# Kernel tuning notes

Hardware: AMD Instinct MI355X
Metric: run time of the kernel (lower is better)

## Reference

```python
import jax, jax.numpy as jnp
import numpy as np

N_NODES = 20000
N_EDGES = 640000
B = 256
GNN_DIM = 256
HID = 512
INNER = 2048
RANK = 512
N_CLASSES = 3
N_GENES = 6640


def _ln(x, s, b, eps=1e-5):
    mu = jnp.mean(x, axis=-1, keepdims=True)
    var = jnp.mean(jnp.square(x - mu), axis=-1, keepdims=True)
    return (x - mu) * jax.lax.rsqrt(var + eps) * s + b


def setup_inputs() -> dict:
    key = jax.random.key(0)
    ks = jax.random.split(key, 16)
    s = 0.02
    return {
        "node_indices": jax.random.randint(ks[0], (B,), 0, N_NODES, dtype=jnp.int32),
        "edge_index": jax.random.randint(ks[1], (2, N_EDGES), 0, N_NODES, dtype=jnp.int32),
        "edge_weight": jax.random.uniform(ks[2], (N_EDGES,), dtype=jnp.float32),
        "partial_emb": jax.random.normal(ks[3], (N_NODES, GNN_DIM), dtype=jnp.float32),
        "oov_emb": jnp.zeros((1, GNN_DIM), jnp.float32),
        "gnn_ln_s": jnp.ones((3, GNN_DIM), jnp.float32),
        "gnn_ln_b": jnp.zeros((3, GNN_DIM), jnp.float32),
        "gnn_w": jax.random.normal(ks[4], (3, GNN_DIM, GNN_DIM), jnp.float32) * s,
        "gnn_b": jnp.zeros((3, GNN_DIM), jnp.float32),
        "post_w": jax.random.normal(ks[5], (GNN_DIM, GNN_DIM), jnp.float32) * s,
        "post_b": jnp.zeros((GNN_DIM,), jnp.float32),
        "pin_w": jax.random.normal(ks[6], (GNN_DIM, HID), jnp.float32) * s,
        "pin_b": jnp.zeros((HID,), jnp.float32),
        "blk_ln_s": jnp.ones((6, HID), jnp.float32),
        "blk_ln_b": jnp.zeros((6, HID), jnp.float32),
        "blk_w1": jax.random.normal(ks[7], (6, HID, INNER), jnp.float32) * s,
        "blk_b1": jnp.zeros((6, INNER), jnp.float32),
        "blk_w2": jax.random.normal(ks[8], (6, INNER, HID), jnp.float32) * s,
        "blk_b2": jnp.zeros((6, HID), jnp.float32),
        "pout_w": jax.random.normal(ks[9], (HID, N_CLASSES * RANK), jnp.float32) * s,
        "pout_b": jnp.zeros((N_CLASSES * RANK,), jnp.float32),
        "out_gene_emb": jax.random.normal(ks[10], (N_GENES, RANK), jnp.float32) * s,
    }


def reference(node_indices, edge_index, edge_weight, partial_emb, oov_emb,
              gnn_ln_s, gnn_ln_b, gnn_w, gnn_b, post_w, post_b,
              pin_w, pin_b, blk_ln_s, blk_ln_b, blk_w1, blk_b1, blk_w2, blk_b2,
              pout_w, pout_b, out_gene_emb):
    n = partial_emb.shape[0]
    src, dst = edge_index[0], edge_index[1]
    # --- trainable GNN tail: 3 layers of (LN -> weighted scatter-sum -> Linear -> ReLU) + residual ---
    x = partial_emb
    for i in range(3):
        h = _ln(x, gnn_ln_s[i], gnn_ln_b[i])
        msg = h[src] * edge_weight[:, None]              # [E, 256] gather (memory-bound)
        agg = jax.ops.segment_sum(msg, dst, num_segments=n)
        h = jax.nn.relu(agg @ gnn_w[i] + gnn_b[i])
        x = h + x
    x = x @ post_w + post_b                              # post_mp
    # --- OOV-safe perturbation embedding lookup ---
    oov = node_indices < 0
    safe = jnp.where(oov, 0, node_indices)
    pert = jnp.where(oov[:, None], oov_emb, x[safe])     # [B, 256]
    # --- bilinear head ---
    h = pert @ pin_w + pin_b
    for i in range(6):
        z = _ln(h, blk_ln_s[i], blk_ln_b[i])
        z = jax.nn.gelu(z @ blk_w1[i] + blk_b1[i], approximate=False)
        h = h + z @ blk_w2[i] + blk_b2[i]                # dropout = identity (eval)
    proj = (h @ pout_w + pout_b).reshape(h.shape[0], N_CLASSES, RANK)
    logits = jnp.einsum('bcr,gr->bcg', proj, out_gene_emb)
    return logits
```

## Files before the change

### kernel.cpp

```cpp
#include <hip/hip_runtime.h>
#include <hip/hip_bf16.h>
#include <math.h>

#define NNODES 20000
#define NEDGES 640000
#define BSZ 256
#define GDIM 256
#define HID 512
#define INNER 2048
#define RANK 512
#define NCLS 3
#define NGENES 6640

typedef __attribute__((ext_vector_type(8))) short bf16x8;
typedef __attribute__((ext_vector_type(4))) float f32x4;

__device__ inline float bf2f(unsigned short u) {
    return __uint_as_float(((unsigned)u) << 16);
}
__device__ inline unsigned short f2bf(float f) {
    unsigned u = __float_as_uint(f);
    u = u + 0x7fff + ((u >> 16) & 1);
    return (unsigned short)(u >> 16);
}

__global__ void hist_k(const int* __restrict__ dst, int* __restrict__ counts, int E) {
    int e = blockIdx.x * 256 + threadIdx.x;
    if (e < E) atomicAdd(&counts[dst[e]], 1);
}

__global__ void scan1_k(const int* __restrict__ counts, int* __restrict__ incl,
                        int* __restrict__ bsums, int n) {
    __shared__ int s[256];
    int i = blockIdx.x * 256 + threadIdx.x;
    int v = (i < n) ? counts[i] : 0;
    s[threadIdx.x] = v;
    __syncthreads();
    for (int off = 1; off < 256; off <<= 1) {
        int t = (threadIdx.x >= off) ? s[threadIdx.x - off] : 0;
        __syncthreads();
        s[threadIdx.x] += t;
        __syncthreads();
    }
    if (i < n) incl[i] = s[threadIdx.x];
    if (threadIdx.x == 255) bsums[blockIdx.x] = s[255];
}

__global__ void scan2_k(const int* __restrict__ bsums, int* __restrict__ boffs, int nb) {
    __shared__ int s[128];
    int tid = threadIdx.x;
    int v = (tid < nb) ? bsums[tid] : 0;
    s[tid] = v;
    __syncthreads();
    for (int off = 1; off < 128; off <<= 1) {
        int t = (tid >= off) ? s[tid - off] : 0;
        __syncthreads();
        s[tid] += t;
        __syncthreads();
    }
    if (tid < nb) boffs[tid] = s[tid] - v;
}

__global__ void scan3_k(const int* __restrict__ incl, const int* __restrict__ counts,
                        const int* __restrict__ boffs, int* __restrict__ row_start,
                        int* __restrict__ cursor, int n) {
    int i = blockIdx.x * 256 + threadIdx.x;
    if (i < n) {
        int st = incl[i] - counts[i] + boffs[blockIdx.x];
        row_start[i] = st;
        cursor[i] = st;
    }
}

__global__ void scatter_k(const int* __restrict__ src, const int* __restrict__ dst,
                          const float* __restrict__ w, int* __restrict__ cursor,
                          int2* __restrict__ ep, int E) {
    int e = blockIdx.x * 256 + threadIdx.x;
    if (e < E) {
        int d = dst[e];
        int p = atomicAdd(&cursor[d], 1);
        ep[p] = make_int2(src[e], __float_as_int(w[e]));
    }
}

__global__ void cvtb_k(const float* __restrict__ X, unsigned short* __restrict__ Y, int n8) {
    int i = blockIdx.x * 256 + threadIdx.x;
    if (i >= n8) return;
    const float4* xp = (const float4*)X;
    float4 a = xp[i * 2], b = xp[i * 2 + 1];
    *(ushort4*)(Y + (size_t)i * 8) = make_ushort4(f2bf(a.x), f2bf(a.y), f2bf(a.z), f2bf(a.w));
    *(ushort4*)(Y + (size_t)i * 8 + 4) = make_ushort4(f2bf(b.x), f2bf(b.y), f2bf(b.z), f2bf(b.w));
}

__global__ void tconv_k(const float* __restrict__ W, unsigned short* __restrict__ WT, int K,
                        int N) {
    __shared__ float s[32][33];
    const float* Wl = W + (size_t)blockIdx.z * K * N;
    unsigned short* WTl = WT + (size_t)blockIdx.z * K * N;
    int k0 = blockIdx.y * 32, n0 = blockIdx.x * 32;
#pragma unroll
    for (int i = 0; i < 4; i++)
        s[threadIdx.y + 8 * i][threadIdx.x] =
            Wl[(size_t)(k0 + threadIdx.y + 8 * i) * N + n0 + threadIdx.x];
    __syncthreads();
#pragma unroll
    for (int i = 0; i < 4; i++)
        WTl[(size_t)(n0 + threadIdx.y + 8 * i) * K + k0 + threadIdx.x] =
            f2bf(s[threadIdx.x][threadIdx.y + 8 * i]);
}

__global__ void lnb_k(const float* __restrict__ X, const float* __restrict__ sc,
                      const float* __restrict__ bi, unsigned short* __restrict__ Y, int M) {
    int row = blockIdx.x * 4 + (threadIdx.x >> 6);
    int lane = threadIdx.x & 63;
    if (row >= M) return;
    float4 v = ((const float4*)(X + (size_t)row * GDIM))[lane];
    float sum = v.x + v.y + v.z + v.w;
#pragma unroll
    for (int off = 32; off >= 1; off >>= 1) sum += __shfl_xor(sum, off);
    float mu = sum / GDIM;
    float a = v.x - mu, b = v.y - mu, c = v.z - mu, d = v.w - mu;
    float sq = a * a + b * b + c * c + d * d;
#pragma unroll
    for (int off = 32; off >= 1; off >>= 1) sq += __shfl_xor(sq, off);
    float rstd = rsqrtf(sq / GDIM + 1e-5f);
    float4 s4 = ((const float4*)sc)[lane];
    float4 b4 = ((const float4*)bi)[lane];
    *(ushort4*)(Y + (size_t)row * GDIM + lane * 4) =
        make_ushort4(f2bf(a * rstd * s4.x + b4.x), f2bf(b * rstd * s4.y + b4.y),
                     f2bf(c * rstd * s4.z + b4.z), f2bf(d * rstd * s4.w + b4.w));
}

__device__ inline void agg_row(int beg, int cnt, int lane, const int2* __restrict__ ep,
                               const unsigned short* __restrict__ H, float& a0, float& a1,
                               float& a2, float& a3) {
    int t = 0;
    for (; t + 16 <= cnt; t += 16) {
        int2 e[16];
#pragma unroll
        for (int u = 0; u < 16; u++) e[u] = ep[beg + t + u];
        ushort4 v[16];
#pragma unroll
        for (int u = 0; u < 16; u++)
            v[u] = *(const ushort4*)(H + (size_t)e[u].x * GDIM + lane * 4);
#pragma unroll
        for (int u = 0; u < 16; u++) {
            float w = __int_as_float(e[u].y);
            a0 = fmaf(bf2f(v[u].x), w, a0);
            a1 = fmaf(bf2f(v[u].y), w, a1);
            a2 = fmaf(bf2f(v[u].z), w, a2);
            a3 = fmaf(bf2f(v[u].w), w, a3);
        }
    }
    for (; t + 4 <= cnt; t += 4) {
        int2 e[4];
#pragma unroll
        for (int u = 0; u < 4; u++) e[u] = ep[beg + t + u];
        ushort4 v[4];
#pragma unroll
        for (int u = 0; u < 4; u++)
            v[u] = *(const ushort4*)(H + (size_t)e[u].x * GDIM + lane * 4);
#pragma unroll
        for (int u = 0; u < 4; u++) {
            float w = __int_as_float(e[u].y);
            a0 = fmaf(bf2f(v[u].x), w, a0);
            a1 = fmaf(bf2f(v[u].y), w, a1);
            a2 = fmaf(bf2f(v[u].z), w, a2);
            a3 = fmaf(bf2f(v[u].w), w, a3);
        }
    }
    for (; t < cnt; t++) {
        int2 e = ep[beg + t];
        float w = __int_as_float(e.y);
        ushort4 v = *(const ushort4*)(H + (size_t)e.x * GDIM + lane * 4);
        a0 = fmaf(bf2f(v.x), w, a0);
        a1 = fmaf(bf2f(v.y), w, a1);
        a2 = fmaf(bf2f(v.z), w, a2);
        a3 = fmaf(bf2f(v.w), w, a3);
    }
}

__global__ void aggb_k(const int* __restrict__ row_start, const int* __restrict__ counts,
                       const int2* __restrict__ ep, const unsigned short* __restrict__ H,
                       unsigned short* __restrict__ AGG, int n) {
    int row = blockIdx.x * 4 + (threadIdx.x >> 6);
    int lane = threadIdx.x & 63;
    if (row >= n) return;
    float a0 = 0.f, a1 = 0.f, a2 = 0.f, a3 = 0.f;
    agg_row(row_start[row], counts[row], lane, ep, H, a0, a1, a2, a3);
    *(ushort4*)(AGG + (size_t)row * GDIM + lane * 4) =
        make_ushort4(f2bf(a0), f2bf(a1), f2bf(a2), f2bf(a3));
}

__global__ void aggsel_k(const int* __restrict__ idx, const int* __restrict__ row_start,
                         const int* __restrict__ counts, const int2* __restrict__ ep,
                         const unsigned short* __restrict__ H, unsigned short* __restrict__ AGG) {
    int b = blockIdx.x * 4 + (threadIdx.x >> 6);
    int lane = threadIdx.x & 63;
    int id = idx[b];
    int row = id < 0 ? 0 : id;
    float a0 = 0.f, a1 = 0.f, a2 = 0.f, a3 = 0.f;
    agg_row(row_start[row], counts[row], lane, ep, H, a0, a1, a2, a3);
    *(ushort4*)(AGG + (size_t)b * GDIM + lane * 4) =
        make_ushort4(f2bf(a0), f2bf(a1), f2bf(a2), f2bf(a3));
}

template <int ACT, bool RES, bool BIAS>
__global__ __launch_bounds__(256) void mgemm_k(const unsigned short* __restrict__ A,
                                               const unsigned short* __restrict__ BT,
                                               const float* __restrict__ bias,
                                               const float* __restrict__ R,
                                               float* __restrict__ C, int M, int N, int K) {
    __shared__ unsigned short As[128 * 32];
    __shared__ unsigned short Bs[128 * 32];
    int m0 = blockIdx.y * 128, n0 = blockIdx.x * 128;
    int tid = threadIdx.x;
    int wave = tid >> 6, lane = tid & 63;
    int wm = (wave >> 1) * 64, wn = (wave & 1) * 64;
    int lrow = lane & 15, lq = lane >> 4;

    f32x4 acc[4][4];
    const f32x4 zz = {0.f, 0.f, 0.f, 0.f};
#pragma unroll
    for (int i = 0; i < 4; i++)
#pragma unroll
        for (int j = 0; j < 4; j++) acc[i][j] = zz;

    int r0 = tid >> 2;
    int q = tid & 3;

    for (int k0 = 0; k0 < K; k0 += 32) {
#pragma unroll
        for (int p = 0; p < 2; p++) {
            int row = r0 + p * 64;
            int gm = m0 + row;
            uint4 va = make_uint4(0, 0, 0, 0);
            if (gm < M) va = *(const uint4*)(A + (size_t)gm * K + k0 + q * 8);
            *(uint4*)&As[row * 32 + q * 8] = va;
            int gn = n0 + row;
            uint4 vb = make_uint4(0, 0, 0, 0);
            if (gn < N) vb = *(const uint4*)(BT + (size_t)gn * K + k0 + q * 8);
            *(uint4*)&Bs[row * 32 + q * 8] = vb;
        }
        __syncthreads();
        bf16x8 af[4], bf[4];
#pragma unroll
        for (int i = 0; i < 4; i++)
            af[i] = *(const bf16x8*)&As[(wm + i * 16 + lrow) * 32 + lq * 8];
#pragma unroll
        for (int j = 0; j < 4; j++)
            bf[j] = *(const bf16x8*)&Bs[(wn + j * 16 + lrow) * 32 + lq * 8];
#pragma unroll
        for (int i = 0; i < 4; i++)
#pragma unroll
            for (int j = 0; j < 4; j++)
                acc[i][j] =
                    __builtin_amdgcn_mfma_f32_16x16x32_bf16(af[i], bf[j], acc[i][j], 0, 0, 0);
        __syncthreads();
    }

#pragma unroll
    for (int i = 0; i < 4; i++) {
#pragma unroll
        for (int j = 0; j < 4; j++) {
            int gn = n0 + wn + j * 16 + lrow;
            if (gn >= N) continue;
            float bv = BIAS ? bias[gn] : 0.f;
#pragma unroll
            for (int r = 0; r < 4; r++) {
                int gm = m0 + wm + i * 16 + lq * 4 + r;
                if (gm >= M) continue;
                float v = acc[i][j][r] + bv;
                if (ACT == 1) v = fmaxf(v, 0.f);
                if (RES) v += R[(size_t)gm * N + gn];
                C[(size_t)gm * N + gn] = v;
            }
        }
    }
}

template <int ACT, int EPI>
__global__ __launch_bounds__(256) void mfull_k(const unsigned short* __restrict__ A,
                                               const unsigned short* __restrict__ BT,
                                               const float* __restrict__ bias,
                                               const int* __restrict__ idx,
                                               const float* __restrict__ aux,
                                               unsigned short* __restrict__ O, int M, int N,
                                               int K) {
    __shared__ unsigned short As[64 * 32];
    __shared__ unsigned short Bs[64 * 32];
    int m0 = blockIdx.y * 64, n0 = blockIdx.x * 64;
    int tid = threadIdx.x;
    int wave = tid >> 6, lane = tid & 63;
    int wm = wave * 16;
    int lrow = lane & 15, lq = lane >> 4;
    f32x4 acc[4];
    const f32x4 zz = {0.f, 0.f, 0.f, 0.f};
#pragma unroll
    for (int j = 0; j < 4; j++) acc[j] = zz;
    int r0 = tid >> 2;
    int q = tid & 3;
    for (int k0 = 0; k0 < K; k0 += 32) {
        *(uint4*)&As[r0 * 32 + q * 8] = *(const uint4*)(A + (size_t)(m0 + r0) * K + k0 + q * 8);
        *(uint4*)&Bs[r0 * 32 + q * 8] = *(const uint4*)(BT + (size_t)(n0 + r0) * K + k0 + q * 8);
        __syncthreads();
        bf16x8 af = *(const bf16x8*)&As[(wm + lrow) * 32 + lq * 8];
#pragma unroll
        for (int j = 0; j < 4; j++) {
            bf16x8 bfr = *(const bf16x8*)&Bs[(j * 16 + lrow) * 32 + lq * 8];
            acc[j] = __builtin_amdgcn_mfma_f32_16x16x32_bf16(af, bfr, acc[j], 0, 0, 0);
        }
        __syncthreads();
    }
#pragma unroll
    for (int j = 0; j < 4; j++) {
        int gn = n0 + j * 16 + lrow;
        float bv = bias[gn];
#pragma unroll
        for (int r = 0; r < 4; r++) {
            int gm = m0 + wm + lq * 4 + r;
            float v = acc[j][r] + bv;
            if (ACT == 1) v = fmaxf(v, 0.f);
            if (ACT == 2) v = 0.5f * v * (1.f + erff(v * 0.70710678118654752f));
            if (EPI == 2) {
                int id = idx[gm];
                int safe = id < 0 ? 0 : id;
                v += aux[(size_t)safe * N + gn];
            }
            if (EPI == 1) {
                if (idx[gm] < 0) v = aux[gn];
            }
            O[(size_t)gm * N + gn] = f2bf(v);
        }
    }
}

__global__ __launch_bounds__(256) void msk_k(const unsigned short* __restrict__ A,
                                             const unsigned short* __restrict__ BT,
                                             float* __restrict__ Cp, int M, int N, int K,
                                             int kchunk) {
    __shared__ unsigned short As[64 * 32];
    __shared__ unsigned short Bs[64 * 32];
    int m0 = blockIdx.y * 64, n0 = blockIdx.x * 64;
    int kbeg = blockIdx.z * kchunk;
    float* C = Cp + (size_t)blockIdx.z * M * N;
    int tid = threadIdx.x;
    int wave = tid >> 6, lane = tid & 63;
    int wm = wave * 16;
    int lrow = lane & 15, lq = lane >> 4;
    f32x4 acc[4];
    const f32x4 zz = {0.f, 0.f, 0.f, 0.f};
#pragma unroll
    for (int j = 0; j < 4; j++) acc[j] = zz;
    int r0 = tid >> 2;
    int q = tid & 3;
    for (int k0 = kbeg; k0 < kbeg + kchunk; k0 += 32) {
        *(uint4*)&As[r0 * 32 + q * 8] = *(const uint4*)(A + (size_t)(m0 + r0) * K + k0 + q * 8);
        *(uint4*)&Bs[r0 * 32 + q * 8] = *(const uint4*)(BT + (size_t)(n0 + r0) * K + k0 + q * 8);
        __syncthreads();
        bf16x8 af = *(const bf16x8*)&As[(wm + lrow) * 32 + lq * 8];
#pragma unroll
        for (int j = 0; j < 4; j++) {
            bf16x8 bfr = *(const bf16x8*)&Bs[(j * 16 + lrow) * 32 + lq * 8];
            acc[j] = __builtin_amdgcn_mfma_f32_16x16x32_bf16(af, bfr, acc[j], 0, 0, 0);
        }
        __syncthreads();
    }
#pragma unroll
    for (int j = 0; j < 4; j++) {
        int gn = n0 + j * 16 + lrow;
#pragma unroll
        for (int r = 0; r < 4; r++) {
            int gm = m0 + wm + lq * 4 + r;
            C[(size_t)gm * N + gn] = acc[j][r];
        }
    }
}

template <bool RESID, bool DO_LN>
__global__ void redln_k(const float* __restrict__ Cp, const float* __restrict__ bias,
                        const float* __restrict__ ln_s, const float* __restrict__ ln_b,
                        float* __restrict__ hbuf, unsigned short* __restrict__ outbf, int S) {
    int row = blockIdx.x * 4 + (threadIdx.x >> 6);
    int lane = threadIdx.x & 63;
    float4 a0 = {0.f, 0.f, 0.f, 0.f}, a1 = a0;
    for (int s = 0; s < S; s++) {
        const float4* pp = (const float4*)(Cp + ((size_t)s * BSZ + row) * HID);
        float4 b0 = pp[lane * 2], b1 = pp[lane * 2 + 1];
        a0.x += b0.x; a0.y += b0.y; a0.z += b0.z; a0.w += b0.w;
        a1.x += b1.x; a1.y += b1.y; a1.z += b1.z; a1.w += b1.w;
    }
    const float4* bb = (const float4*)bias;
    float4 c0 = bb[lane * 2], c1 = bb[lane * 2 + 1];
    a0.x += c0.x; a0.y += c0.y; a0.z += c0.z; a0.w += c0.w;
    a1.x += c1.x; a1.y += c1.y; a1.z += c1.z; a1.w += c1.w;
    float4* hp = (float4*)(hbuf + (size_t)row * HID);
    if (RESID) {
        float4 r0 = hp[lane * 2], r1 = hp[lane * 2 + 1];
        a0.x += r0.x; a0.y += r0.y; a0.z += r0.z; a0.w += r0.w;
        a1.x += r1.x; a1.y += r1.y; a1.z += r1.z; a1.w += r1.w;
    }
    hp[lane * 2] = a0;
    hp[lane * 2 + 1] = a1;
    unsigned short* op = outbf + (size_t)row * HID;
    if (DO_LN) {
        float sum = a0.x + a0.y + a0.z + a0.w + a1.x + a1.y + a1.z + a1.w;
#pragma unroll
        for (int off = 32; off >= 1; off >>= 1) sum += __shfl_xor(sum, off);
        float mu = sum / HID;
        float d0 = a0.x - mu, d1 = a0.y - mu, d2 = a0.z - mu, d3 = a0.w - mu;
        float d4 = a1.x - mu, d5 = a1.y - mu, d6 = a1.z - mu, d7 = a1.w - mu;
        float sq = d0 * d0 + d1 * d1 + d2 * d2 + d3 * d3 + d4 * d4 + d5 * d5 + d6 * d6 + d7 * d7;
#pragma unroll
        for (int off = 32; off >= 1; off >>= 1) sq += __shfl_xor(sq, off);
        float rstd = rsqrtf(sq / HID + 1e-5f);
        const float4* sp = (const float4*)ln_s;
        const float4* bp = (const float4*)ln_b;
        float4 s0 = sp[lane * 2], s1 = sp[lane * 2 + 1];
        float4 t0 = bp[lane * 2], t1 = bp[lane * 2 + 1];
        *(ushort4*)(op + lane * 8) =
            make_ushort4(f2bf(d0 * rstd * s0.x + t0.x), f2bf(d1 * rstd * s0.y + t0.y),
                         f2bf(d2 * rstd * s0.z + t0.z), f2bf(d3 * rstd * s0.w + t0.w));
        *(ushort4*)(op + lane * 8 + 4) =
            make_ushort4(f2bf(d4 * rstd * s1.x + t1.x), f2bf(d5 * rstd * s1.y + t1.y),
                         f2bf(d6 * rstd * s1.z + t1.z), f2bf(d7 * rstd * s1.w + t1.w));
    } else {
        *(ushort4*)(op + lane * 8) = make_ushort4(f2bf(a0.x), f2bf(a0.y), f2bf(a0.z), f2bf(a0.w));
        *(ushort4*)(op + lane * 8 + 4) =
            make_ushort4(f2bf(a1.x), f2bf(a1.y), f2bf(a1.z), f2bf(a1.w));
    }
}

extern "C" void kernel_launch(void* const* d_in, const int* in_sizes, int n_in,
                              void* d_out, int out_size, void* d_ws, size_t ws_size,
                              hipStream_t stream) {
    const int* node_indices = (const int*)d_in[0];
    const int* edge_src = (const int*)d_in[1];
    const int* edge_dst = edge_src + NEDGES;
    const float* edge_w = (const float*)d_in[2];
    const float* partial_emb = (const float*)d_in[3];
    const float* oov_emb = (const float*)d_in[4];
    const float* gnn_ln_s = (const float*)d_in[5];
    const float* gnn_ln_b = (const float*)d_in[6];
    const float* gnn_w = (const float*)d_in[7];
    const float* gnn_b = (const float*)d_in[8];
    const float* post_w = (const float*)d_in[9];
    const float* post_b = (const float*)d_in[10];
    const float* pin_w = (const float*)d_in[11];
    const float* pin_b = (const float*)d_in[12];
    const float* blk_ln_s = (const float*)d_in[13];
    const float* blk_ln_b = (const float*)d_in[14];
    const float* blk_w1 = (const float*)d_in[15];
    const float* blk_b1 = (const float*)d_in[16];
    const float* blk_w2 = (const float*)d_in[17];
    const float* blk_b2 = (const float*)d_in[18];
    const float* pout_w = (const float*)d_in[19];
    const float* pout_b = (const float*)d_in[20];
    const float* gene = (const float*)d_in[21];
    float* out = (float*)d_out;

    char* p = (char*)d_ws;
    auto alloc = [&](size_t bytes) {
        char* r = p;
        p += (bytes + 255) & ~(size_t)255;
        return r;
    };
    int* counts = (int*)alloc(NNODES * 4);
    int* incl = (int*)alloc(NNODES * 4);
    int* bsums = (int*)alloc(128 * 4);
    int* boffs = (int*)alloc(128 * 4);
    int* row_start = (int*)alloc(NNODES * 4);
    int* cursor = (int*)alloc(NNODES * 4);
    int2* epack = (int2*)alloc((size_t)NEDGES * 8);
    float* part = (float*)alloc((size_t)NNODES * GDIM * 4);
    unsigned short* ln_bf = (unsigned short*)part;
    unsigned short* aggbf = (unsigned short*)((char*)part + (size_t)NNODES * GDIM * 2);
    float* xa = (float*)alloc((size_t)NNODES * GDIM * 4);
    float* xb = (float*)alloc((size_t)NNODES * GDIM * 4);
    float* hbuf = (float*)alloc((size_t)BSZ * HID * 4);
    unsigned short* aggselb = (unsigned short*)alloc((size_t)BSZ * GDIM * 2);
    unsigned short* pertinbf = (unsigned short*)alloc((size_t)BSZ * GDIM * 2);
    unsigned short* pertbf = (unsigned short*)alloc((size_t)BSZ * GDIM * 2);
    unsigned short* zlnbf = (unsigned short*)alloc((size_t)BSZ * HID * 2);
    unsigned short* z1bf = (unsigned short*)alloc((size_t)BSZ * INNER * 2);
    unsigned short* hbufbf = (unsigned short*)alloc((size_t)BSZ * HID * 2);
    unsigned short* projb = (unsigned short*)alloc((size_t)BSZ * NCLS * RANK * 2);
    unsigned short* gnnT = (unsigned short*)alloc((size_t)3 * GDIM * GDIM * 2);
    unsigned short* postT = (unsigned short*)alloc((size_t)GDIM * GDIM * 2);
    unsigned short* pinT = (unsigned short*)alloc((size_t)HID * GDIM * 2);
    unsigned short* w1T = (unsigned short*)alloc((size_t)6 * INNER * HID * 2);
    unsigned short* w2T = (unsigned short*)alloc((size_t)6 * HID * INNER * 2);
    unsigned short* poutT = (unsigned short*)alloc((size_t)NCLS * RANK * HID * 2);
    unsigned short* geneb = (unsigned short*)alloc((size_t)NGENES * RANK * 2);

    const int EB = (NEDGES + 255) / 256;
    const int NB = (NNODES + 255) / 256;

    tconv_k<<<dim3(GDIM / 32, GDIM / 32, 3), dim3(32, 8), 0, stream>>>(gnn_w, gnnT, GDIM, GDIM);
    tconv_k<<<dim3(GDIM / 32, GDIM / 32, 1), dim3(32, 8), 0, stream>>>(post_w, postT, GDIM, GDIM);
    tconv_k<<<dim3(HID / 32, GDIM / 32, 1), dim3(32, 8), 0, stream>>>(pin_w, pinT, GDIM, HID);
    tconv_k<<<dim3(INNER / 32, HID / 32, 6), dim3(32, 8), 0, stream>>>(blk_w1, w1T, HID, INNER);
    tconv_k<<<dim3(HID / 32, INNER / 32, 6), dim3(32, 8), 0, stream>>>(blk_w2, w2T, INNER, HID);
    tconv_k<<<dim3((NCLS * RANK) / 32, HID / 32, 1), dim3(32, 8), 0, stream>>>(pout_w, poutT, HID,
                                                                               NCLS * RANK);
    cvtb_k<<<(NGENES * RANK / 8 + 255) / 256, 256, 0, stream>>>(gene, geneb, NGENES * RANK / 8);

    hipMemsetAsync(counts, 0, NNODES * 4, stream);
    hist_k<<<EB, 256, 0, stream>>>(edge_dst, counts, NEDGES);
    scan1_k<<<NB, 256, 0, stream>>>(counts, incl, bsums, NNODES);
    scan2_k<<<1, 128, 0, stream>>>(bsums, boffs, NB);
    scan3_k<<<NB, 256, 0, stream>>>(incl, counts, boffs, row_start, cursor, NNODES);
    scatter_k<<<EB, 256, 0, stream>>>(edge_src, edge_dst, edge_w, cursor, epack, NEDGES);

    const float* x_in = partial_emb;
    float* bufs[2] = {xa, xb};
    for (int i = 0; i < 2; i++) {
        lnb_k<<<(NNODES + 3) / 4, 256, 0, stream>>>(x_in, gnn_ln_s + i * GDIM,
                                                    gnn_ln_b + i * GDIM, ln_bf, NNODES);
        aggb_k<<<(NNODES + 3) / 4, 256, 0, stream>>>(row_start, counts, epack, ln_bf, aggbf,
                                                     NNODES);
        float* x_out = bufs[i];
        mgemm_k<1, true, true><<<dim3(GDIM / 128, (NNODES + 127) / 128), 256, 0, stream>>>(
            aggbf, gnnT + (size_t)i * GDIM * GDIM, gnn_b + i * GDIM, x_in, x_out, NNODES, GDIM,
            GDIM);
        x_in = x_out;
    }
    lnb_k<<<(NNODES + 3) / 4, 256, 0, stream>>>(xb, gnn_ln_s + 2 * GDIM, gnn_ln_b + 2 * GDIM,
                                                ln_bf, NNODES);
    aggsel_k<<<BSZ / 4, 256, 0, stream>>>(node_indices, row_start, counts, epack, ln_bf, aggselb);
    mfull_k<1, 2><<<dim3(GDIM / 64, BSZ / 64), 256, 0, stream>>>(
        aggselb, gnnT + (size_t)2 * GDIM * GDIM, gnn_b + 2 * GDIM, node_indices, xb, pertinbf,
        BSZ, GDIM, GDIM);

    mfull_k<0, 1><<<dim3(GDIM / 64, BSZ / 64), 256, 0, stream>>>(
        pertinbf, postT, post_b, node_indices, oov_emb, pertbf, BSZ, GDIM, GDIM);

    msk_k<<<dim3(HID / 64, BSZ / 64, 4), 256, 0, stream>>>(pertbf, pinT, part, BSZ, HID, GDIM,
                                                           GDIM / 4);
    redln_k<false, true><<<BSZ / 4, 256, 0, stream>>>(part, pin_b, blk_ln_s, blk_ln_b, hbuf,
                                                      zlnbf, 4);

    for (int i = 0; i < 6; i++) {
        mfull_k<2, 0><<<dim3(INNER / 64, BSZ / 64), 256, 0, stream>>>(
            zlnbf, w1T + (size_t)i * INNER * HID, blk_b1 + i * INNER, nullptr, nullptr, z1bf, BSZ,
            INNER, HID);
        msk_k<<<dim3(HID / 64, BSZ / 64, 8), 256, 0, stream>>>(
            z1bf, w2T + (size_t)i * HID * INNER, part, BSZ, HID, INNER, INNER / 8);
        if (i < 5) {
            redln_k<true, true><<<BSZ / 4, 256, 0, stream>>>(
                part, blk_b2 + i * HID, blk_ln_s + (i + 1) * HID, blk_ln_b + (i + 1) * HID, hbuf,
                zlnbf, 8);
        } else {
            redln_k<true, false><<<BSZ / 4, 256, 0, stream>>>(part, blk_b2 + i * HID, nullptr,
                                                              nullptr, hbuf, hbufbf, 8);
        }
    }

    mfull_k<0, 0><<<dim3((NCLS * RANK) / 64, BSZ / 64), 256, 0, stream>>>(
        hbufbf, poutT, pout_b, nullptr, nullptr, projb, BSZ, NCLS * RANK, HID);

    mgemm_k<0, false, false><<<dim3((NGENES + 127) / 128, (BSZ * NCLS) / 128), 256, 0, stream>>>(
        projb, geneb, nullptr, nullptr, out, BSZ * NCLS, NGENES, RANK);
}
```

Before: 610.6 us.

## Fuse bilinear head into persistent grid-synced kernel and merge weight conversions

The roughly twenty separate launches of the MLP head (input projection, six residual blocks of GEMM, split-K reduce and LayerNorm, then the output projection) become one persistent 256-block kernel. Its phases are separated by a software grid barrier built on atomics, and it uses new 32x64 register-prefetched GEMM tiles, with the second block GEMM split 4 ways along K instead of 8. The seven transpose/convert launches for weights and gene embeddings are also merged into a single kernel that dispatches on block index. The aim is to remove per-launch overhead and tail gaps, at the cost of spin-barrier latency and correctness that depends on all 256 blocks being resident at once.

Result: slower. 1.001 ms (+63.9%).

```diff
diff --git a/kernel.cpp b/kernel.cpp
--- a/kernel.cpp
+++ b/kernel.cpp
@@ -83,30 +83,68 @@
     }
 }
 
-__global__ void cvtb_k(const float* __restrict__ X, unsigned short* __restrict__ Y, int n8) {
-    int i = blockIdx.x * 256 + threadIdx.x;
-    if (i >= n8) return;
-    const float4* xp = (const float4*)X;
-    float4 a = xp[i * 2], b = xp[i * 2 + 1];
-    *(ushort4*)(Y + (size_t)i * 8) = make_ushort4(f2bf(a.x), f2bf(a.y), f2bf(a.z), f2bf(a.w));
-    *(ushort4*)(Y + (size_t)i * 8 + 4) = make_ushort4(f2bf(b.x), f2bf(b.y), f2bf(b.z), f2bf(b.w));
-}
-
-__global__ void tconv_k(const float* __restrict__ W, unsigned short* __restrict__ WT, int K,
-                        int N) {
+__global__ void convall_k(const float* __restrict__ gnn_w, const float* __restrict__ post_w,
+                          const float* __restrict__ pin_w, const float* __restrict__ blk_w1,
+                          const float* __restrict__ blk_w2, const float* __restrict__ pout_w,
+                          const float* __restrict__ gene, unsigned short* __restrict__ gnnT,
+                          unsigned short* __restrict__ postT, unsigned short* __restrict__ pinT,
+                          unsigned short* __restrict__ w1T, unsigned short* __restrict__ w2T,
+                          unsigned short* __restrict__ poutT,
+                          unsigned short* __restrict__ geneb) {
+    int b = blockIdx.x;
+    if (b >= 13440) {
+        int t = b - 13440;
+        const float4* xp = (const float4*)gene;
+        int i = t * 512 + threadIdx.x * 2;
+        float4 a = xp[i], c = xp[i + 1];
+        *(ushort4*)(geneb + (size_t)i * 4) =
+            make_ushort4(f2bf(a.x), f2bf(a.y), f2bf(a.z), f2bf(a.w));
+        *(ushort4*)(geneb + (size_t)i * 4 + 4) =
+            make_ushort4(f2bf(c.x), f2bf(c.y), f2bf(c.z), f2bf(c.w));
+        return;
+    }
+    const float* W;
+    unsigned short* WT;
+    int K, N, tile;
+    if (b < 192) {
+        int l = b >> 6;
+        tile = b & 63;
+        W = gnn_w + (size_t)l * GDIM * GDIM;
+        WT = gnnT + (size_t)l * GDIM * GDIM;
+        K = GDIM; N = GDIM;
+    } else if (b < 256) {
+        tile = b - 192; W = post_w; WT = postT; K = GDIM; N = GDIM;
+    } else if (b < 384) {
+        tile = b - 256; W = pin_w; WT = pinT; K = GDIM; N = HID;
+    } else if (b < 6528) {
+        int t = b - 384;
+        int l = t >> 10;
+        tile = t & 1023;
+        W = blk_w1 + (size_t)l * HID * INNER;
+        WT = w1T + (size_t)l * INNER * HID;
+        K = HID; N = INNER;
+    } else if (b < 12672) {
+        int t = b - 6528;
+        int l = t >> 10;
+        tile = t & 1023;
+        W = blk_w2 + (size_t)l * INNER * HID;
+        WT = w2T + (size_t)l * HID * INNER;
+        K = INNER; N = HID;
+    } else {
+        tile = b - 12672; W = pout_w; WT = poutT; K = HID; N = NCLS * RANK;
+    }
     __shared__ float s[32][33];
-    const float* Wl = W + (size_t)blockIdx.z * K * N;
-    unsigned short* WTl = WT + (size_t)blockIdx.z * K * N;
-    int k0 = blockIdx.y * 32, n0 = blockIdx.x * 32;
+    int ntx = N >> 5;
+    int k0 = (tile / ntx) << 5;
+    int n0 = (tile % ntx) << 5;
+    int tx = threadIdx.x & 31, ty = threadIdx.x >> 5;
 #pragma unroll
     for (int i = 0; i < 4; i++)
-        s[threadIdx.y + 8 * i][threadIdx.x] =
-            Wl[(size_t)(k0 + threadIdx.y + 8 * i) * N + n0 + threadIdx.x];
+        s[ty + 8 * i][tx] = W[(size_t)(k0 + ty + 8 * i) * N + n0 + tx];
     __syncthreads();
 #pragma unroll
     for (int i = 0; i < 4; i++)
-        WTl[(size_t)(n0 + threadIdx.y + 8 * i) * K + k0 + threadIdx.x] =
-            f2bf(s[threadIdx.x][threadIdx.y + 8 * i]);
+        WT[(size_t)(n0 + ty + 8 * i) * K + k0 + tx] = f2bf(s[tx][ty + 8 * i]);
 }
 
 __global__ void lnb_k(const float* __restrict__ X, const float* __restrict__ sc,
@@ -335,56 +373,113 @@
     }
 }
 
-__global__ __launch_bounds__(256) void msk_k(const unsigned short* __restrict__ A,
-                                             const unsigned short* __restrict__ BT,
-                                             float* __restrict__ Cp, int M, int N, int K,
-                                             int kchunk) {
-    __shared__ unsigned short As[64 * 32];
-    __shared__ unsigned short Bs[64 * 32];
-    int m0 = blockIdx.y * 64, n0 = blockIdx.x * 64;
-    int kbeg = blockIdx.z * kchunk;
-    float* C = Cp + (size_t)blockIdx.z * M * N;
+
+#define HGRID 256
+#define LDP 72
+
+__device__ inline void gsync(int* bar, int target) {
+    __syncthreads();
+    if (threadIdx.x == 0) {
+        __threadfence();
+        __hip_atomic_fetch_add(bar, 1, __ATOMIC_RELEASE, __HIP_MEMORY_SCOPE_AGENT);
+        while (__hip_atomic_load(bar, __ATOMIC_ACQUIRE, __HIP_MEMORY_SCOPE_AGENT) < target)
+            __builtin_amdgcn_s_sleep(2);
+    }
+    __syncthreads();
+}
+
+__device__ inline void gemm32x64(const unsigned short* __restrict__ A, int lda,
+                                 const unsigned short* __restrict__ BT, int ldb, int m0, int n0,
+                                 int kbeg, int kcnt, unsigned short* As, unsigned short* Bs,
+                                 f32x4 acc[2]) {
     int tid = threadIdx.x;
     int wave = tid >> 6, lane = tid & 63;
-    int wm = wave * 16;
+    int wm = (wave >> 1) * 16, wn = (wave & 1) * 32;
     int lrow = lane & 15, lq = lane >> 4;
-    f32x4 acc[4];
-    const f32x4 zz = {0.f, 0.f, 0.f, 0.f};
-#pragma unroll
-    for (int j = 0; j < 4; j++) acc[j] = zz;
-    int r0 = tid >> 2;
-    int q = tid & 3;
-    for (int k0 = kbeg; k0 < kbeg + kchunk; k0 += 32) {
-        *(uint4*)&As[r0 * 32 + q * 8] = *(const uint4*)(A + (size_t)(m0 + r0) * K + k0 + q * 8);
-        *(uint4*)&Bs[r0 * 32 + q * 8] = *(const uint4*)(BT + (size_t)(n0 + r0) * K + k0 + q * 8);
-        __syncthreads();
-        bf16x8 af = *(const bf16x8*)&As[(wm + lrow) * 32 + lq * 8];
-#pragma unroll
-        for (int j = 0; j < 4; j++) {
-            bf16x8 bfr = *(const bf16x8*)&Bs[(j * 16 + lrow) * 32 + lq * 8];
-            acc[j] = __builtin_amdgcn_mfma_f32_16x16x32_bf16(af, bfr, acc[j], 0, 0, 0);
-        }
-        __syncthreads();
-    }
-#pragma unroll
-    for (int j = 0; j < 4; j++) {
-        int gn = n0 + j * 16 + lrow;
+    int rb = tid >> 2, qb = tid & 3;
+    int ra = rb & 31;
+    const unsigned short* bp = BT + (size_t)(n0 + rb) * ldb + kbeg + qb * 16;
+    const unsigned short* ap = A + (size_t)(m0 + ra) * lda + kbeg + qb * 16;
+    uint4 vb0 = *(const uint4*)bp, vb1 = *(const uint4*)(bp + 8);
+    uint4 va0 = {0, 0, 0, 0}, va1 = {0, 0, 0, 0};
+    if (tid < 128) {
+        va0 = *(const uint4*)ap;
+        va1 = *(const uint4*)(ap + 8);
+    }
+    for (int k0 = 0; k0 < kcnt; k0 += 64) {
+        *(uint4*)&Bs[rb * LDP + qb * 16] = vb0;
+        *(uint4*)&Bs[rb * LDP + qb * 16 + 8] = vb1;
+        if (tid < 128) {
+            *(uint4*)&As[ra * LDP + qb * 16] = va0;
+            *(uint4*)&As[ra * LDP + qb * 16 + 8] = va1;
+        }
+        __syncthreads();
+        if (k0 + 64 < kcnt) {
+            vb0 = *(const uint4*)(bp + k0 + 64);
+            vb1 = *(const uint4*)(bp + k0 + 72);
+            if (tid < 128) {
+                va0 = *(const uint4*)(ap + k0 + 64);
+                va1 = *(const uint4*)(ap + k0 + 72);
+            }
+        }
+#pragma unroll
+        for (int kk = 0; kk < 2; kk++) {
+            bf16x8 af = *(const bf16x8*)&As[(wm + lrow) * LDP + kk * 32 + lq * 8];
+#pragma unroll
+            for (int j = 0; j < 2; j++) {
+                bf16x8 bfr = *(const bf16x8*)&Bs[(wn + j * 16 + lrow) * LDP + kk * 32 + lq * 8];
+                acc[j] = __builtin_amdgcn_mfma_f32_16x16x32_bf16(af, bfr, acc[j], 0, 0, 0);
+            }
+        }
+        __syncthreads();
+    }
+}
+
+template <int ACT>
+__device__ inline void epi32x64_bf(const f32x4 acc[2], const float* __restrict__ bias,
+                                   unsigned short* __restrict__ O, int ldo, int m0, int n0) {
+    int tid = threadIdx.x, wave = tid >> 6, lane = tid & 63;
+    int wm = (wave >> 1) * 16, wn = (wave & 1) * 32;
+    int lrow = lane & 15, lq = lane >> 4;
+#pragma unroll
+    for (int j = 0; j < 2; j++) {
+        int gn = n0 + wn + j * 16 + lrow;
+        float bv = bias[gn];
 #pragma unroll
         for (int r = 0; r < 4; r++) {
             int gm = m0 + wm + lq * 4 + r;
-            C[(size_t)gm * N + gn] = acc[j][r];
+            float v = acc[j][r] + bv;
+            if (ACT == 2) v = 0.5f * v * (1.f + erff(v * 0.70710678118654752f));
+            O[(size_t)gm * ldo + gn] = f2bf(v);
+        }
+    }
+}
+
+__device__ inline void epi32x64_f32(const f32x4 acc[2], float* __restrict__ C, int ldo, int m0,
+                                    int n0) {
+    int tid = threadIdx.x, wave = tid >> 6, lane = tid & 63;
+    int wm = (wave >> 1) * 16, wn = (wave & 1) * 32;
+    int lrow = lane & 15, lq = lane >> 4;
+#pragma unroll
+    for (int j = 0; j < 2; j++) {
+        int gn = n0 + wn + j * 16 + lrow;
+#pragma unroll
+        for (int r = 0; r < 4; r++) {
+            int gm = m0 + wm + lq * 4 + r;
+            C[(size_t)gm * ldo + gn] = acc[j][r];
         }
     }
 }
 
 template <bool RESID, bool DO_LN>
-__global__ void redln_k(const float* __restrict__ Cp, const float* __restrict__ bias,
-                        const float* __restrict__ ln_s, const float* __restrict__ ln_b,
-                        float* __restrict__ hbuf, unsigned short* __restrict__ outbf, int S) {
+__device__ inline void redln_dev(const float* __restrict__ Cp, const float* __restrict__ bias,
+                                 const float* __restrict__ ln_s, const float* __restrict__ ln_b,
+                                 float* __restrict__ hbuf, unsigned short* __restrict__ outbf) {
     int row = blockIdx.x * 4 + (threadIdx.x >> 6);
     int lane = threadIdx.x & 63;
     float4 a0 = {0.f, 0.f, 0.f, 0.f}, a1 = a0;
-    for (int s = 0; s < S; s++) {
+#pragma unroll
+    for (int s = 0; s < 4; s++) {
         const float4* pp = (const float4*)(Cp + ((size_t)s * BSZ + row) * HID);
         float4 b0 = pp[lane * 2], b1 = pp[lane * 2 + 1];
         a0.x += b0.x; a0.y += b0.y; a0.z += b0.z; a0.w += b0.w;
@@ -415,9 +510,9 @@
         for (int off = 32; off >= 1; off >>= 1) sq += __shfl_xor(sq, off);
         float rstd = rsqrtf(sq / HID + 1e-5f);
         const float4* sp = (const float4*)ln_s;
-        const float4* bp = (const float4*)ln_b;
+        const float4* bp2 = (const float4*)ln_b;
         float4 s0 = sp[lane * 2], s1 = sp[lane * 2 + 1];
-        float4 t0 = bp[lane * 2], t1 = bp[lane * 2 + 1];
+        float4 t0 = bp2[lane * 2], t1 = bp2[lane * 2 + 1];
         *(ushort4*)(op + lane * 8) =
             make_ushort4(f2bf(d0 * rstd * s0.x + t0.x), f2bf(d1 * rstd * s0.y + t0.y),
                          f2bf(d2 * rstd * s0.z + t0.z), f2bf(d3 * rstd * s0.w + t0.w));
@@ -428,6 +523,72 @@
         *(ushort4*)(op + lane * 8) = make_ushort4(f2bf(a0.x), f2bf(a0.y), f2bf(a0.z), f2bf(a0.w));
         *(ushort4*)(op + lane * 8 + 4) =
             make_ushort4(f2bf(a1.x), f2bf(a1.y), f2bf(a1.z), f2bf(a1.w));
+    }
+}
+
+__global__ __launch_bounds__(256) void head_k(
+    const unsigned short* __restrict__ pertbf, const unsigned short* __restrict__ pinT,
+    const float* __restrict__ pin_b, const float* __restrict__ blk_ln_s,
+    const float* __restrict__ blk_ln_b, const unsigned short* __restrict__ w1T,
+    const float* __restrict__ blk_b1, const unsigned short* __restrict__ w2T,
+    const float* __restrict__ blk_b2, const unsigned short* __restrict__ poutT,
+    const float* __restrict__ pout_b, float* __restrict__ hbuf,
+    unsigned short* __restrict__ zlnbf, unsigned short* __restrict__ z1bf,
+    float* __restrict__ part, unsigned short* __restrict__ hbufbf,
+    unsigned short* __restrict__ projb, int* __restrict__ bar) {
+    __shared__ unsigned short As[32 * LDP];
+    __shared__ unsigned short Bs[64 * LDP];
+    int b = blockIdx.x;
+    int ph = 0;
+    f32x4 acc[2];
+    const f32x4 zz = {0.f, 0.f, 0.f, 0.f};
+
+    {
+        int s = b >> 6, t = b & 63;
+        int m0 = (t >> 3) * 32, n0 = (t & 7) * 64;
+        acc[0] = zz; acc[1] = zz;
+        gemm32x64(pertbf, GDIM, pinT, GDIM, m0, n0, s * 64, 64, As, Bs, acc);
+        epi32x64_f32(acc, part + (size_t)s * BSZ * HID, HID, m0, n0);
+    }
+    gsync(bar, ++ph * HGRID);
+    if (b < 64) redln_dev<false, true>(part, pin_b, blk_ln_s, blk_ln_b, hbuf, zlnbf);
+    gsync(bar, ++ph * HGRID);
+
+    for (int i = 0; i < 6; i++) {
+        {
+            int m0 = (b >> 5) * 32, n0 = (b & 31) * 64;
+            acc[0] = zz; acc[1] = zz;
+            gemm32x64(zlnbf, HID, w1T + (size_t)i * INNER * HID, HID, m0, n0, 0, HID, As, Bs,
+                      acc);
+            epi32x64_bf<2>(acc, blk_b1 + (size_t)i * INNER, z1bf, INNER, m0, n0);
+        }
+        gsync(bar, ++ph * HGRID);
+        {
+            int s = b >> 6, t = b & 63;
+            int m0 = (t >> 3) * 32, n0 = (t & 7) * 64;
+            acc[0] = zz; acc[1] = zz;
+            gemm32x64(z1bf, INNER, w2T + (size_t)i * HID * INNER, INNER, m0, n0, s * 512, 512,
+                      As, Bs, acc);
+            epi32x64_f32(acc, part + (size_t)s * BSZ * HID, HID, m0, n0);
+        }
+        gsync(bar, ++ph * HGRID);
+        if (b < 64) {
+            if (i < 5)
+                redln_dev<true, true>(part, blk_b2 + (size_t)i * HID,
+                                      blk_ln_s + (size_t)(i + 1) * HID,
+                                      blk_ln_b + (size_t)(i + 1) * HID, hbuf, zlnbf);
+            else
+                redln_dev<true, false>(part, blk_b2 + (size_t)i * HID, nullptr, nullptr, hbuf,
+                                       hbufbf);
+        }
+        gsync(bar, ++ph * HGRID);
+    }
+
+    if (b < 192) {
+        int m0 = (b / 24) * 32, n0 = (b % 24) * 64;
+        acc[0] = zz; acc[1] = zz;
+        gemm32x64(hbufbf, HID, poutT, HID, m0, n0, 0, HID, As, Bs, acc);
+        epi32x64_bf<0>(acc, pout_b, projb, NCLS * RANK, m0, n0);
     }
 }
 
@@ -492,20 +653,16 @@
     unsigned short* w2T = (unsigned short*)alloc((size_t)6 * HID * INNER * 2);
     unsigned short* poutT = (unsigned short*)alloc((size_t)NCLS * RANK * HID * 2);
     unsigned short* geneb = (unsigned short*)alloc((size_t)NGENES * RANK * 2);
+    int* bar = (int*)alloc(256);
 
     const int EB = (NEDGES + 255) / 256;
     const int NB = (NNODES + 255) / 256;
 
-    tconv_k<<<dim3(GDIM / 32, GDIM / 32, 3), dim3(32, 8), 0, stream>>>(gnn_w, gnnT, GDIM, GDIM);
-    tconv_k<<<dim3(GDIM / 32, GDIM / 32, 1), dim3(32, 8), 0, stream>>>(post_w, postT, GDIM, GDIM);
-    tconv_k<<<dim3(HID / 32, GDIM / 32, 1), dim3(32, 8), 0, stream>>>(pin_w, pinT, GDIM, HID);
-    tconv_k<<<dim3(INNER / 32, HID / 32, 6), dim3(32, 8), 0, stream>>>(blk_w1, w1T, HID, INNER);
-    tconv_k<<<dim3(HID / 32, INNER / 32, 6), dim3(32, 8), 0, stream>>>(blk_w2, w2T, INNER, HID);
-    tconv_k<<<dim3((NCLS * RANK) / 32, HID / 32, 1), dim3(32, 8), 0, stream>>>(pout_w, poutT, HID,
-                                                                               NCLS * RANK);
-    cvtb_k<<<(NGENES * RANK / 8 + 255) / 256, 256, 0, stream>>>(gene, geneb, NGENES * RANK / 8);
+    convall_k<<<15100, 256, 0, stream>>>(gnn_w, post_w, pin_w, blk_w1, blk_w2, pout_w, gene,
+                                         gnnT, postT, pinT, w1T, w2T, poutT, geneb);
 
     hipMemsetAsync(counts, 0, NNODES * 4, stream);
+    hipMemsetAsync(bar, 0, 4, stream);
     hist_k<<<EB, 256, 0, stream>>>(edge_dst, counts, NEDGES);
     scan1_k<<<NB, 256, 0, stream>>>(counts, incl, bsums, NNODES);
     scan2_k<<<1, 128, 0, stream>>>(bsums, boffs, NB);
@@ -535,29 +692,9 @@
     mfull_k<0, 1><<<dim3(GDIM / 64, BSZ / 64), 256, 0, stream>>>(
         pertinbf, postT, post_b, node_indices, oov_emb, pertbf, BSZ, GDIM, GDIM);
 
-    msk_k<<<dim3(HID / 64, BSZ / 64, 4), 256, 0, stream>>>(pertbf, pinT, part, BSZ, HID, GDIM,
-                                                           GDIM / 4);
-    redln_k<false, true><<<BSZ / 4, 256, 0, stream>>>(part, pin_b, blk_ln_s, blk_ln_b, hbuf,
-                                                      zlnbf, 4);
-
-    for (int i = 0; i < 6; i++) {
-        mfull_k<2, 0><<<dim3(INNER / 64, BSZ / 64), 256, 0, stream>>>(
-            zlnbf, w1T + (size_t)i * INNER * HID, blk_b1 + i * INNER, nullptr, nullptr, z1bf, BSZ,
-            INNER, HID);
-        msk_k<<<dim3(HID / 64, BSZ / 64, 8), 256, 0, stream>>>(
-            z1bf, w2T + (size_t)i * HID * INNER, part, BSZ, HID, INNER, INNER / 8);
-        if (i < 5) {
-            redln_k<true, true><<<BSZ / 4, 256, 0, stream>>>(
-                part, blk_b2 + i * HID, blk_ln_s + (i + 1) * HID, blk_ln_b + (i + 1) * HID, hbuf,
-                zlnbf, 8);
-        } else {
-            redln_k<true, false><<<BSZ / 4, 256, 0, stream>>>(part, blk_b2 + i * HID, nullptr,
-                                                              nullptr, hbuf, hbufbf, 8);
-        }
-    }
-
-    mfull_k<0, 0><<<dim3((NCLS * RANK) / 64, BSZ / 64), 256, 0, stream>>>(
-        hbufbf, poutT, pout_b, nullptr, nullptr, projb, BSZ, NCLS * RANK, HID);
+    head_k<<<HGRID, 256, 0, stream>>>(pertbf, pinT, pin_b, blk_ln_s, blk_ln_b, w1T, blk_b1, w2T,
+                                      blk_b2, poutT, pout_b, hbuf, zlnbf, z1bf, part, hbufbf,
+                                      projb, bar);
 
     mgemm_k<0, false, false><<<dim3((NGENES + 127) / 128, (BSZ * NCLS) / 128), 256, 0, stream>>>(
         projb, geneb, nullptr, nullptr, out, BSZ * NCLS, NGENES, RANK);
```
